# Performance work log

Measured on AMD Instinct MI355X. Metric: run time of the kernel, lower is better.

The kernel has to match this reference:

```python
import jax, jax.numpy as jnp
import numpy as np

D_MODEL = 1024
N_HEADS = 16
HEAD_DIM = D_MODEL // N_HEADS  # 64
TOP_K = 64
EPS = 1e-12  # matches F.normalize eps


def setup_inputs() -> dict:
    key = jax.random.key(0)
    ks = jax.random.split(key, 6)
    s = 0.02
    def w(k):
        return jax.random.normal(k, (D_MODEL, D_MODEL), jnp.float32) * s
    zb = jnp.zeros((D_MODEL,), jnp.float32)
    # x: (B, T, d_model); T must equal d_model (see compress_proj constraint)
    x = jax.random.normal(ks[0], (2, 1024, D_MODEL), jnp.float32)
    return {
        "x": x,
        "Wq": w(ks[1]), "bq": zb,
        "Wk": w(ks[2]), "bk": zb,
        "Wv": w(ks[3]), "bv": zb,
        "Wo": w(ks[4]), "bo": zb,
        "Wc": w(ks[5]), "bc": zb,  # compress_proj (applied along time axis)
    }


def _l2norm(a):
    n = jnp.linalg.norm(a, axis=-1, keepdims=True)
    return a / jnp.maximum(n, EPS)


def reference(x, Wq, bq, Wk, bk, Wv, bv, Wo, bo, Wc, bc):
    B, T, Dm = x.shape
    H, hd = N_HEADS, HEAD_DIM

    def proj(W, b):
        return (x @ W.T + b).reshape(B, T, H, hd).transpose(0, 2, 1, 3)  # (B,H,T,hd)

    Q = proj(Wq, bq)
    K = proj(Wk, bk)
    V = proj(Wv, bv)

    # compress_kv with compress_ratio=1: compress_proj acts on the (transposed)
    # time axis, so K_comp[b,h,c,d] = sum_t K[b,h,t,d] * Wc[c,t] + bc[c]
    K_comp = jnp.einsum('bhtd,ct->bhcd', K, Wc) + bc[None, None, :, None]
    V_comp = jnp.einsum('bhtd,ct->bhcd', V, Wc) + bc[None, None, :, None]

    # lightning indexer: cosine similarity + top-k over compressed slots
    sim = jnp.einsum('bhtd,bhcd->bhtc', _l2norm(Q), _l2norm(K_comp))
    topk_idx = jax.lax.top_k(sim, TOP_K)[1]  # (B,H,T,K)

    bi = jnp.arange(B)[:, None, None, None]
    hi = jnp.arange(H)[None, :, None, None]
    K_sel = K_comp[bi, hi, topk_idx]  # (B,H,T,K,hd)
    V_sel = V_comp[bi, hi, topk_idx]

    scores = jnp.einsum('bhtd,bhtkd->bhtk', Q, K_sel) / float(np.sqrt(hd))
    attn = jax.nn.softmax(scores, axis=-1)
    out = jnp.einsum('bhtk,bhtkd->bhtd', attn, V_sel)  # (B,H,T,hd)
    out = out.transpose(0, 2, 1, 3).reshape(B, T, Dm)
    return out @ Wo.T + bo
```

## Files before the change

kernel.cpp:

```cpp
#include <hip/hip_runtime.h>
#include <type_traits>


#define DEVI __device__ __forceinline__

constexpr int Tn = 1024;
constexpr int Cn = 1024;
constexpr int Hn = 16;

typedef short bf16x8 __attribute__((ext_vector_type(8)));
typedef float f32x4 __attribute__((ext_vector_type(4)));
typedef double f64x4 __attribute__((ext_vector_type(4)));

DEVI int wsumi(int v)   { for (int m = 1; m < 64; m <<= 1) v += __shfl_xor(v, m); return v; }
DEVI int wmini(int v)   { for (int m = 1; m < 64; m <<= 1) { int o = __shfl_xor(v, m); v = o < v ? o : v; } return v; }
DEVI float wfmax(float v){ for (int m = 1; m < 64; m <<= 1) v = fmaxf(v, __shfl_xor(v, m)); return v; }
DEVI float wfsum(float v){ for (int m = 1; m < 64; m <<= 1) v += __shfl_xor(v, m); return v; }

DEVI unsigned long long mapd(double x) {
  unsigned long long b = (unsigned long long)__double_as_longlong(x);
  return (b >> 63) ? ~b : (b | 0x8000000000000000ull);
}

DEVI unsigned short f2bf_rne(float x) {
  unsigned u = __float_as_uint(x);
  u += 0x7fffu + ((u >> 16) & 1u);
  return (unsigned short)(u >> 16);
}
struct BfPair { short hi, lo; };
DEVI BfPair split2(float x) {
  unsigned short h = f2bf_rne(x);
  float hf = __uint_as_float(((unsigned)h) << 16);
  BfPair r;
  r.hi = (short)h;
  r.lo = (short)f2bf_rne(x - hf);
  return r;
}

template <typename OUTT, bool BTRANS, int BIASMODE>
DEVI void f64_body(float* AsB, float* BsB,
    const float* Ab, const float* Bb, const float* bias, OUTT* Cb,
    int Kd, int lda, int ldb, int ldc, int m0, int n0)
{
  const int tid = threadIdx.x;
  const int lane = tid & 63, w = tid >> 6;
  const int wr = w >> 1, wc = w & 1;
  const int l15 = lane & 15, l4 = lane >> 4;

  f64x4 zz = {0.0, 0.0, 0.0, 0.0};
  f64x4 p1 = __builtin_amdgcn_mfma_f64_16x16x4f64(1.0, (double)l15, zz, 0, 0, 0);
  f64x4 p2 = __builtin_amdgcn_mfma_f64_16x16x4f64((double)l15, 1.0, zz, 0, 0, 0);
  int a1 = 1, b1 = 1, c1 = 1, a2 = 1, b2 = 1, c2 = 1;
#pragma unroll
  for (int rr = 0; rr < 4; ++rr) {
    a1 &= (p1[rr] == 4.0 * l15);
    b1 &= (p1[rr] == 4.0 * (l4 * 4 + rr));
    c1 &= (p1[rr] == 4.0 * (l4 + 4 * rr));
    a2 &= (p2[rr] == 4.0 * (l4 * 4 + rr));
    b2 &= (p2[rr] == 4.0 * (l4 + 4 * rr));
    c2 &= (p2[rr] == 4.0 * l15);
  }
  a1 = __all(a1); b1 = __all(b1); c1 = __all(c1);
  a2 = __all(a2); b2 = __all(b2); c2 = __all(c2);
  int dmap = 0, useM = 1;
  if      (a1 && a2) dmap = 0;
  else if (a1 && b2) dmap = 1;
  else if (b1 && c2) dmap = 2;
  else if (c1 && c2) dmap = 3;
  else useM = 0;

  f64x4 acc[2][2];
#pragma unroll
  for (int i = 0; i < 2; ++i)
#pragma unroll
    for (int j = 0; j < 2; ++j) acc[i][j] = (f64x4){0.0, 0.0, 0.0, 0.0};

  const int sm = tid >> 2, skf = tid & 3;
  const int bkl = tid >> 4, bnf = tid & 15;

  const int nT = Kd >> 5;
  float4 a0_, a1_, b0_, b1_;

  auto LOADT = [&](int k0) {
    a0_ = *(const float4*)(Ab + (size_t)(m0 + sm) * lda + k0 + 4 * skf);
    a1_ = *(const float4*)(Ab + (size_t)(m0 + sm) * lda + k0 + 16 + 4 * skf);
    if (BTRANS) {
      b0_ = *(const float4*)(Bb + (size_t)(n0 + sm) * ldb + k0 + 4 * skf);
      b1_ = *(const float4*)(Bb + (size_t)(n0 + sm) * ldb + k0 + 16 + 4 * skf);
    } else {
      b0_ = *(const float4*)(Bb + (size_t)(k0 + bkl) * ldb + n0 + 4 * bnf);
      b1_ = *(const float4*)(Bb + (size_t)(k0 + 16 + bkl) * ldb + n0 + 4 * bnf);
    }
  };
  auto WRITET = [&](int buf) {
    float* As = AsB + buf * 2304;
    float* Bs = BsB + buf * 2304;
    As[(4 * skf + 0) * 72 + sm] = a0_.x; As[(4 * skf + 1) * 72 + sm] = a0_.y;
    As[(4 * skf + 2) * 72 + sm] = a0_.z; As[(4 * skf + 3) * 72 + sm] = a0_.w;
    As[(16 + 4 * skf + 0) * 72 + sm] = a1_.x; As[(16 + 4 * skf + 1) * 72 + sm] = a1_.y;
    As[(16 + 4 * skf + 2) * 72 + sm] = a1_.z; As[(16 + 4 * skf + 3) * 72 + sm] = a1_.w;
    if (BTRANS) {
      Bs[(4 * skf + 0) * 72 + sm] = b0_.x; Bs[(4 * skf + 1) * 72 + sm] = b0_.y;
      Bs[(4 * skf + 2) * 72 + sm] = b0_.z; Bs[(4 * skf + 3) * 72 + sm] = b0_.w;
      Bs[(16 + 4 * skf + 0) * 72 + sm] = b1_.x; Bs[(16 + 4 * skf + 1) * 72 + sm] = b1_.y;
      Bs[(16 + 4 * skf + 2) * 72 + sm] = b1_.z; Bs[(16 + 4 * skf + 3) * 72 + sm] = b1_.w;
    } else {
      *(float4*)&Bs[bkl * 72 + 4 * bnf] = b0_;
      *(float4*)&Bs[(16 + bkl) * 72 + 4 * bnf] = b1_;
    }
  };

  LOADT(0);
  WRITET(0);
  __syncthreads();

  for (int kt = 0; kt < nT; ++kt) {
    const int cur = kt & 1;
    if (kt + 1 < nT) LOADT((kt + 1) * 32);

    const float* As = AsB + cur * 2304;
    const float* Bs = BsB + cur * 2304;
    if (useM) {
#pragma unroll
      for (int kq = 0; kq < 8; ++kq) {
        int kk = kq * 4 + l4;
        double a0  = (double)As[kk * 72 + wr * 32 + l15];
        double a1v = (double)As[kk * 72 + wr * 32 + 16 + l15];
        double b0  = (double)Bs[kk * 72 + wc * 32 + l15];
        double b1v = (double)Bs[kk * 72 + wc * 32 + 16 + l15];
        acc[0][0] = __builtin_amdgcn_mfma_f64_16x16x4f64(a0,  b0,  acc[0][0], 0, 0, 0);
        acc[0][1] = __builtin_amdgcn_mfma_f64_16x16x4f64(a0,  b1v, acc[0][1], 0, 0, 0);
        acc[1][0] = __builtin_amdgcn_mfma_f64_16x16x4f64(a1v, b0,  acc[1][0], 0, 0, 0);
        acc[1][1] = __builtin_amdgcn_mfma_f64_16x16x4f64(a1v, b1v, acc[1][1], 0, 0, 0);
      }
    } else {
#pragma unroll
      for (int k = 0; k < 32; ++k) {
        double bv0 = (double)Bs[k * 72 + wc * 32 + l15];
        double bv1 = (double)Bs[k * 72 + wc * 32 + 16 + l15];
#pragma unroll
        for (int fr = 0; fr < 2; ++fr)
#pragma unroll
          for (int rr = 0; rr < 4; ++rr) {
            double av = (double)As[k * 72 + wr * 32 + fr * 16 + l4 * 4 + rr];
            acc[fr][0][rr] += av * bv0;
            acc[fr][1][rr] += av * bv1;
          }
      }
    }

    if (kt + 1 < nT) WRITET(cur ^ 1);
    __syncthreads();
  }

#pragma unroll
  for (int fr = 0; fr < 2; ++fr)
#pragma unroll
    for (int fc = 0; fc < 2; ++fc)
#pragma unroll
      for (int rr = 0; rr < 4; ++rr) {
        int ri, ci;
        if (!useM || dmap == 0) { ri = l4 * 4 + rr; ci = l15; }
        else if (dmap == 1)     { ri = l4 + 4 * rr; ci = l15; }
        else if (dmap == 2)     { ri = l15; ci = l4 * 4 + rr; }
        else                    { ri = l15; ci = l4 + 4 * rr; }
        int row = m0 + wr * 32 + fr * 16 + ri;
        int col = n0 + wc * 32 + fc * 16 + ci;
        double v = acc[fr][fc][rr];
        if constexpr (std::is_same<OUTT, double>::value) {
          Cb[(size_t)row * ldc + col] = v;
        } else {
          float s = (float)v;
          float cb = (BIASMODE == 1) ? bias[col] : 0.f;
          float rb = (BIASMODE == 2) ? bias[row] : 0.f;
          ((float*)Cb)[(size_t)row * ldc + col] = s + cb + rb;
        }
      }
}

template <bool BTRANS, int BIASMODE>
DEVI void bf16_body(short* AhB, short* AlB, short* BhB, short* BlB,
    const float* A, const float* Bz, const float* bias, float* Cz,
    int Kd, int lda, int ldb, int ldc, int m0, int n0)
{
  const int tid = threadIdx.x;
  const int lane = tid & 63, w = tid >> 6;
  const int wr = w >> 1, wc = w & 1;
  const int r16 = lane & 15, kg = lane >> 4;

  f32x4 acc[2][2];
#pragma unroll
  for (int i = 0; i < 2; ++i)
#pragma unroll
    for (int j = 0; j < 2; ++j) acc[i][j] = (f32x4){0.f, 0.f, 0.f, 0.f};

  const int row = tid >> 2, kseg = tid & 3;
  const int gcol = tid & 63, gks = tid >> 6;

  const int nT = Kd >> 5;
  float4 pa0, pa1, pb0, pb1;
  float gb[8];

  auto LOADT = [&](int k0) {
    pa0 = *(const float4*)(A + (size_t)(m0 + row) * lda + k0 + kseg * 8);
    pa1 = *(const float4*)(A + (size_t)(m0 + row) * lda + k0 + kseg * 8 + 4);
    if (BTRANS) {
      pb0 = *(const float4*)(Bz + (size_t)(n0 + row) * ldb + k0 + kseg * 8);
      pb1 = *(const float4*)(Bz + (size_t)(n0 + row) * ldb + k0 + kseg * 8 + 4);
    } else {
#pragma unroll
      for (int j = 0; j < 8; ++j)
        gb[j] = Bz[(size_t)(k0 + gks * 8 + j) * ldb + n0 + gcol];
    }
  };
  auto WRITET = [&](int buf) {
    {
      BfPair q0 = split2(pa0.x), q1 = split2(pa0.y), q2 = split2(pa0.z), q3 = split2(pa0.w);
      BfPair q4 = split2(pa1.x), q5 = split2(pa1.y), q6 = split2(pa1.z), q7 = split2(pa1.w);
      bf16x8 h = {q0.hi, q1.hi, q2.hi, q3.hi, q4.hi, q5.hi, q6.hi, q7.hi};
      bf16x8 l = {q0.lo, q1.lo, q2.lo, q3.lo, q4.lo, q5.lo, q6.lo, q7.lo};
      int idx = (kseg * 64 + row) * 8;
      *(bf16x8*)&AhB[buf * 2048 + idx] = h;
      *(bf16x8*)&AlB[buf * 2048 + idx] = l;
    }
    if (BTRANS) {
      BfPair q0 = split2(pb0.x), q1 = split2(pb0.y), q2 = split2(pb0.z), q3 = split2(pb0.w);
      BfPair q4 = split2(pb1.x), q5 = split2(pb1.y), q6 = split2(pb1.z), q7 = split2(pb1.w);
      bf16x8 h = {q0.hi, q1.hi, q2.hi, q3.hi, q4.hi, q5.hi, q6.hi, q7.hi};
      bf16x8 l = {q0.lo, q1.lo, q2.lo, q3.lo, q4.lo, q5.lo, q6.lo, q7.lo};
      int idx = (kseg * 64 + row) * 8;
      *(bf16x8*)&BhB[buf * 2048 + idx] = h;
      *(bf16x8*)&BlB[buf * 2048 + idx] = l;
    } else {
      short hv[8], lv[8];
#pragma unroll
      for (int j = 0; j < 8; ++j) {
        BfPair p = split2(gb[j]);
        hv[j] = p.hi; lv[j] = p.lo;
      }
      bf16x8 h = {hv[0], hv[1], hv[2], hv[3], hv[4], hv[5], hv[6], hv[7]};
      bf16x8 l = {lv[0], lv[1], lv[2], lv[3], lv[4], lv[5], lv[6], lv[7]};
      int idx = (gks * 64 + gcol) * 8;
      *(bf16x8*)&BhB[buf * 2048 + idx] = h;
      *(bf16x8*)&BlB[buf * 2048 + idx] = l;
    }
  };

  LOADT(0);
  WRITET(0);
  __syncthreads();

  for (int kt = 0; kt < nT; ++kt) {
    const int cur = kt & 1;
    if (kt + 1 < nT) LOADT((kt + 1) * 32);

    bf16x8 ah[2], al[2], bh[2], bl[2];
#pragma unroll
    for (int f = 0; f < 2; ++f) {
      int ia = (kg * 64 + wr * 32 + f * 16 + r16) * 8;
      int ib = (kg * 64 + wc * 32 + f * 16 + r16) * 8;
      ah[f] = *(const bf16x8*)&AhB[cur * 2048 + ia];
      al[f] = *(const bf16x8*)&AlB[cur * 2048 + ia];
      bh[f] = *(const bf16x8*)&BhB[cur * 2048 + ib];
      bl[f] = *(const bf16x8*)&BlB[cur * 2048 + ib];
    }
#pragma unroll
    for (int fr = 0; fr < 2; ++fr)
#pragma unroll
      for (int fc = 0; fc < 2; ++fc) {
        f32x4 c = acc[fr][fc];
        c = __builtin_amdgcn_mfma_f32_16x16x32_bf16(al[fr], bh[fc], c, 0, 0, 0);
        c = __builtin_amdgcn_mfma_f32_16x16x32_bf16(ah[fr], bl[fc], c, 0, 0, 0);
        c = __builtin_amdgcn_mfma_f32_16x16x32_bf16(ah[fr], bh[fc], c, 0, 0, 0);
        acc[fr][fc] = c;
      }

    if (kt + 1 < nT) WRITET(cur ^ 1);
    __syncthreads();
  }

#pragma unroll
  for (int fr = 0; fr < 2; ++fr)
#pragma unroll
    for (int fc = 0; fc < 2; ++fc) {
      int col = n0 + wc * 32 + fc * 16 + r16;
      float cb = (BIASMODE == 1) ? bias[col] : 0.f;
#pragma unroll
      for (int rr = 0; rr < 4; ++rr) {
        int rw = m0 + wr * 32 + fr * 16 + kg * 4 + rr;
        float rb = (BIASMODE == 2) ? bias[rw] : 0.f;
        Cz[(size_t)rw * ldc + col] = acc[fr][fc][rr] + cb + rb;
      }
    }
}

__global__ __launch_bounds__(256) void projQKV_k(
    const float* __restrict__ x,
    const float* __restrict__ Wq, const float* __restrict__ Wk,
    const float* __restrict__ Wv,
    const float* __restrict__ bq, const float* __restrict__ bk,
    const float* __restrict__ bv,
    float* __restrict__ Q, float* __restrict__ Kf, float* __restrict__ Vf)
{
  __shared__ __align__(16) float S1[2 * 2304];
  __shared__ __align__(16) float S2[2 * 2304];
  const int m0 = blockIdx.y * 64, n0 = blockIdx.x * 64;
  if (blockIdx.z < 2) {
    const float* W = blockIdx.z ? Wk : Wq;
    const float* b = blockIdx.z ? bk : bq;
    float* C = blockIdx.z ? Kf : Q;
    f64_body<float, true, 1>(S1, S2, x, W, b, C, 1024, 1024, 1024, 1024, m0, n0);
  } else {
    bf16_body<true, 1>((short*)S1, (short*)S1 + 4096,
                       (short*)S2, (short*)S2 + 4096,
                       x, Wv, bv, Vf, 1024, 1024, 1024, 1024, m0, n0);
  }
}

__global__ __launch_bounds__(256) void compKV_k(
    const float* __restrict__ Wc, const float* __restrict__ Kf,
    const float* __restrict__ Vf, const float* __restrict__ bc,
    float* __restrict__ Kc, float* __restrict__ Vc)
{
  __shared__ __align__(16) float S1[2 * 2304];
  __shared__ __align__(16) float S2[2 * 2304];
  const int m0 = blockIdx.y * 64, n0 = blockIdx.x * 64;
  const size_t M1 = (size_t)1024 * 1024;
  if (blockIdx.z < 2) {
    f64_body<float, false, 2>(S1, S2, Wc, Kf + blockIdx.z * M1, bc,
                              Kc + blockIdx.z * M1, 1024, 1024, 1024, 1024, m0, n0);
  } else {
    int zb = blockIdx.z - 2;
    bf16_body<false, 2>((short*)S1, (short*)S1 + 4096,
                        (short*)S2, (short*)S2 + 4096,
                        Wc, Vf + zb * M1, bc, Vc + zb * M1,
                        1024, 1024, 1024, 1024, m0, n0);
  }
}

__global__ __launch_bounds__(256) void dotsim_k(
    const float* __restrict__ Q, const float* __restrict__ Kc,
    double* __restrict__ dotp, int group_base)
{
  __shared__ __align__(16) float S1[2 * 2304];
  __shared__ __align__(16) float S2[2 * 2304];
  const int m0 = blockIdx.y * 64, n0 = blockIdx.x * 64;
  int pair = group_base + (int)blockIdx.z;
  int bb = pair >> 4, hh = pair & 15;
  const float* Ab = Q + ((size_t)bb * Tn) * 1024 + (size_t)hh * 64;
  const float* Bb = Kc + ((size_t)bb * Cn) * 1024 + (size_t)hh * 64;
  double* Cb = dotp + (size_t)blockIdx.z * Tn * Cn;
  f64_body<double, true, 0>(S1, S2, Ab, Bb, nullptr, Cb, 64, 1024, 1024, 1024, m0, n0);
}

__global__ __launch_bounds__(256) void wo_k(
    const float* __restrict__ at, const float* __restrict__ Wo,
    const float* __restrict__ bo, float* __restrict__ out)
{
  __shared__ __align__(16) float S1[2 * 2304];
  __shared__ __align__(16) float S2[2 * 2304];
  const int m0 = blockIdx.y * 64, n0 = blockIdx.x * 64;
  bf16_body<true, 1>((short*)S1, (short*)S1 + 4096,
                     (short*)S2, (short*)S2 + 4096,
                     at, Wo, bo, out, 1024, 1024, 1024, 1024, m0, n0);
}

__global__ __launch_bounds__(256) void kn_k2(const float* __restrict__ Kc,
                                             double* __restrict__ kn)
{
  int idx = (int)blockIdx.x * 256 + (int)threadIdx.x;
  int c = idx & 1023;
  int p = idx >> 10;
  int b = p >> 4, h = p & 15;
  const float* row = Kc + ((size_t)(b * 1024 + c)) * 1024 + h * 64;
  double s = 0.0;
  for (int d = 0; d < 64; ++d) { double v = (double)row[d]; s += v * v; }
  kn[(size_t)p * 1024 + c] = 1.0 / fmax(sqrt(s), 1e-12);
}

__global__ __launch_bounds__(256) void topk_attn_k(
    const double* __restrict__ dotb, const double* __restrict__ kn,
    const float* __restrict__ Vc, float* __restrict__ attnout, int group_base)
{
  __shared__ int sC[4][64];
  __shared__ float sD[4][64];

  const int lane = threadIdx.x & 63, wv = threadIdx.x >> 6;
  const int g = (int)blockIdx.x >> 8;
  const int t = ((int)blockIdx.x & 255) * 4 + wv;
  const int pair = group_base + g;
  const int bb = pair >> 4, hh = pair & 15;

  const double* drow = dotb + ((size_t)g * Tn + t) * (size_t)Cn;
  const double* knr  = kn + ((size_t)(bb * Hn + hh)) * Cn;

  double dv[16];
  unsigned long long u[16];
#pragma unroll
  for (int j = 0; j < 8; ++j) {
    double2 dd = *(const double2*)(drow + j * 128 + 2 * lane);
    double2 kk = *(const double2*)(knr  + j * 128 + 2 * lane);
    dv[2 * j] = dd.x; dv[2 * j + 1] = dd.y;
    u[2 * j]     = mapd(dd.x * kk.x);
    u[2 * j + 1] = mapd(dd.y * kk.y);
  }
  unsigned hi[16];
#pragma unroll
  for (int i = 0; i < 16; ++i) hi[i] = (unsigned)(u[i] >> 32);

  unsigned TH = 0;
  for (int bit = 31; bit >= 0; --bit) {
    unsigned Tc = TH | (1u << bit);
    int c = 0;
#pragma unroll
    for (int i = 0; i < 16; ++i) c += (hi[i] >= Tc);
    if (wsumi(c) >= 64) TH = Tc;
  }
  int mhi = 0;
#pragma unroll
  for (int i = 0; i < 16; ++i) mhi += (hi[i] > TH);
  mhi = wsumi(mhi);
  const int need1 = 64 - mhi;
  unsigned TL = 0;
  for (int bit = 31; bit >= 0; --bit) {
    unsigned Tc = TL | (1u << bit);
    int c = 0;
#pragma unroll
    for (int i = 0; i < 16; ++i) c += (hi[i] == TH && (unsigned)u[i] >= Tc);
    if (wsumi(c) >= need1) TL = Tc;
  }
  const unsigned long long V64 = ((unsigned long long)TH << 32) | TL;

  int base = 0;
#pragma unroll
  for (int i = 0; i < 16; ++i) {
    const int cix = 128 * (i >> 1) + 2 * lane + (i & 1);
    bool sel = (u[i] > V64);
    unsigned long long mk = __ballot(sel);
    if (sel) {
      int r = __popcll(mk & ((1ull << lane) - 1ull));
      sC[wv][base + r] = cix;
      sD[wv][base + r] = (float)dv[i];
    }
    base += __popcll(mk);
  }
  const int need = 64 - base;
  unsigned taken = 0;
  for (int r = 0; r < need; ++r) {
    int mn = 0x7fffffff;
#pragma unroll
    for (int i = 0; i < 16; ++i) {
      int cix = 128 * (i >> 1) + 2 * lane + (i & 1);
      if (u[i] == V64 && !((taken >> i) & 1u)) mn = mn < cix ? mn : cix;
    }
    mn = wmini(mn);
#pragma unroll
    for (int i = 0; i < 16; ++i) {
      int cix = 128 * (i >> 1) + 2 * lane + (i & 1);
      if (u[i] == V64 && !((taken >> i) & 1u) && cix == mn) {
        taken |= 1u << i;
        sC[wv][base + r] = mn;
        sD[wv][base + r] = (float)dv[i];
      }
    }
  }
  __syncthreads();

  int ck = sC[wv][lane];
  float sc = sD[wv][lane] * 0.125f;
  float mx = wfmax(sc);
  float w = expf(sc - mx);
  float sw = wfsum(w);
  w /= sw;

  const float* Vb = Vc + (size_t)bb * ((size_t)Cn * 1024) + hh * 64 + lane;
  float acc = 0.f;
#pragma unroll 4
  for (int k = 0; k < 64; ++k) {
    int c = __shfl(ck, k);
    float wk = __shfl(w, k);
    acc = fmaf(wk, Vb[(size_t)c * 1024], acc);
  }
  attnout[((size_t)(bb * Tn + t)) * 1024 + hh * 64 + lane] = acc;
}

extern "C" void kernel_launch(void* const* d_in, const int* in_sizes, int n_in,
                              void* d_out, int out_size, void* d_ws, size_t ws_size,
                              hipStream_t stream)
{
  const float* x  = (const float*)d_in[0];
  const float* Wq = (const float*)d_in[1];
  const float* bq = (const float*)d_in[2];
  const float* Wk = (const float*)d_in[3];
  const float* bk = (const float*)d_in[4];
  const float* Wv = (const float*)d_in[5];
  const float* bv = (const float*)d_in[6];
  const float* Wo = (const float*)d_in[7];
  const float* bo = (const float*)d_in[8];
  const float* Wc = (const float*)d_in[9];
  const float* bc = (const float*)d_in[10];
  float* out = (float*)d_out;

  const size_t NE = (size_t)2048 * 1024;
  float* Q   = (float*)d_ws;
  float* Kf  = Q + NE;
  float* Vf  = Kf + NE;
  float* Kc  = Vf + NE;
  float* Vc  = Kc + NE;
  float* at  = Vc + NE;
  double* kn = (double*)(at + NE);
  double* tail = kn + 32768;

  const size_t fixedB = 6 * NE * 4 + 32768 * 8;
  const size_t dotPairB = (size_t)Tn * Cn * 8;
  if (ws_size < fixedB) return;

  size_t rem = ws_size - fixedB;
  double* dotp; int G;
  if      (rem >= 32 * dotPairB) { G = 32; dotp = tail; }
  else if (rem >= 16 * dotPairB) { G = 16; dotp = tail; }
  else if (rem >=  8 * dotPairB) { G = 8;  dotp = tail; }
  else if (rem >=  4 * dotPairB) { G = 4;  dotp = tail; }
  else if (rem >=  2 * dotPairB) { G = 2;  dotp = tail; }
  else { G = 2; dotp = (double*)Kf; }

  dim3 blk(256, 1, 1);

  projQKV_k<<<dim3(16, 32, 3), blk, 0, stream>>>(
      x, Wq, Wk, Wv, bq, bk, bv, Q, Kf, Vf);

  compKV_k<<<dim3(16, 16, 4), blk, 0, stream>>>(Wc, Kf, Vf, bc, Kc, Vc);

  kn_k2<<<dim3(128), blk, 0, stream>>>(Kc, kn);

  for (int gb = 0; gb < 32; gb += G) {
    dotsim_k<<<dim3(16, 16, G), blk, 0, stream>>>(Q, Kc, dotp, gb);
    topk_attn_k<<<dim3(256 * G), blk, 0, stream>>>(dotp, kn, Vc, at, gb);
  }

  wo_k<<<dim3(16, 32, 1), blk, 0, stream>>>(at, Wo, bo, out);
}
```

Measured before the change: 810.2 us.

## Software-pipeline dot-similarity GEMM with top-k attention in a fused kernel

Adds a combined kernel whose first 1024 blocks compute the f64 dot-similarity tiles for the next group of four (batch, head) pairs, while the remaining blocks run top-k selection and attention on the previous group from a double buffer. GEMM-bound and latency-bound work now share the GPU instead of running as alternating launches. The cost is a smaller group size, about eight launches where the largest workspace allowed two, and less cache locality. Small workspaces keep the old path, without its 8/16/32 group sizes.

```diff
diff --git a/kernel.cpp b/kernel.cpp
--- a/kernel.cpp
+++ b/kernel.cpp
@@ -294,6 +294,111 @@
     }
 }
 
+DEVI void topk_body(const double* __restrict__ dotb, const double* __restrict__ kn,
+                    const float* __restrict__ Vc, float* __restrict__ attnout,
+                    int flat, int group_base, int* sCp, float* sDp)
+{
+  const int lane = threadIdx.x & 63, wv = threadIdx.x >> 6;
+  const int g = flat >> 8;
+  const int t = (flat & 255) * 4 + wv;
+  const int pair = group_base + g;
+  const int bb = pair >> 4, hh = pair & 15;
+
+  const double* drow = dotb + ((size_t)g * Tn + t) * (size_t)Cn;
+  const double* knr  = kn + ((size_t)(bb * Hn + hh)) * Cn;
+  int* sC = sCp + wv * 64;
+  float* sD = sDp + wv * 64;
+
+  double dv[16];
+  unsigned long long u[16];
+#pragma unroll
+  for (int j = 0; j < 8; ++j) {
+    double2 dd = *(const double2*)(drow + j * 128 + 2 * lane);
+    double2 kk = *(const double2*)(knr  + j * 128 + 2 * lane);
+    dv[2 * j] = dd.x; dv[2 * j + 1] = dd.y;
+    u[2 * j]     = mapd(dd.x * kk.x);
+    u[2 * j + 1] = mapd(dd.y * kk.y);
+  }
+  unsigned hi[16];
+#pragma unroll
+  for (int i = 0; i < 16; ++i) hi[i] = (unsigned)(u[i] >> 32);
+
+  unsigned TH = 0;
+  for (int bit = 31; bit >= 0; --bit) {
+    unsigned Tc = TH | (1u << bit);
+    int c = 0;
+#pragma unroll
+    for (int i = 0; i < 16; ++i) c += (hi[i] >= Tc);
+    if (wsumi(c) >= 64) TH = Tc;
+  }
+  int mhi = 0;
+#pragma unroll
+  for (int i = 0; i < 16; ++i) mhi += (hi[i] > TH);
+  mhi = wsumi(mhi);
+  const int need1 = 64 - mhi;
+  unsigned TL = 0;
+  for (int bit = 31; bit >= 0; --bit) {
+    unsigned Tc = TL | (1u << bit);
+    int c = 0;
+#pragma unroll
+    for (int i = 0; i < 16; ++i) c += (hi[i] == TH && (unsigned)u[i] >= Tc);
+    if (wsumi(c) >= need1) TL = Tc;
+  }
+  const unsigned long long V64 = ((unsigned long long)TH << 32) | TL;
+
+  int base = 0;
+#pragma unroll
+  for (int i = 0; i < 16; ++i) {
+    const int cix = 128 * (i >> 1) + 2 * lane + (i & 1);
+    bool sel = (u[i] > V64);
+    unsigned long long mk = __ballot(sel);
+    if (sel) {
+      int r = __popcll(mk & ((1ull << lane) - 1ull));
+      sC[base + r] = cix;
+      sD[base + r] = (float)dv[i];
+    }
+    base += __popcll(mk);
+  }
+  const int need = 64 - base;
+  unsigned taken = 0;
+  for (int r = 0; r < need; ++r) {
+    int mn = 0x7fffffff;
+#pragma unroll
+    for (int i = 0; i < 16; ++i) {
+      int cix = 128 * (i >> 1) + 2 * lane + (i & 1);
+      if (u[i] == V64 && !((taken >> i) & 1u)) mn = mn < cix ? mn : cix;
+    }
+    mn = wmini(mn);
+#pragma unroll
+    for (int i = 0; i < 16; ++i) {
+      int cix = 128 * (i >> 1) + 2 * lane + (i & 1);
+      if (u[i] == V64 && !((taken >> i) & 1u) && cix == mn) {
+        taken |= 1u << i;
+        sC[base + r] = mn;
+        sD[base + r] = (float)dv[i];
+      }
+    }
+  }
+  __syncthreads();
+
+  int ck = sC[lane];
+  float sc = sD[lane] * 0.125f;
+  float mx = wfmax(sc);
+  float w = expf(sc - mx);
+  float sw = wfsum(w);
+  w /= sw;
+
+  const float* Vb = Vc + (size_t)bb * ((size_t)Cn * 1024) + hh * 64 + lane;
+  float acc = 0.f;
+#pragma unroll 4
+  for (int k = 0; k < 64; ++k) {
+    int c = __shfl(ck, k);
+    float wk = __shfl(w, k);
+    acc = fmaf(wk, Vb[(size_t)c * 1024], acc);
+  }
+  attnout[((size_t)(bb * Tn + t)) * 1024 + hh * 64 + lane] = acc;
+}
+
 __global__ __launch_bounds__(256) void projQKV_k(
     const float* __restrict__ x,
     const float* __restrict__ Wq, const float* __restrict__ Wk,
@@ -353,16 +458,36 @@
   f64_body<double, true, 0>(S1, S2, Ab, Bb, nullptr, Cb, 64, 1024, 1024, 1024, m0, n0);
 }
 
-__global__ __launch_bounds__(256) void wo_k(
-    const float* __restrict__ at, const float* __restrict__ Wo,
-    const float* __restrict__ bo, float* __restrict__ out)
+__global__ __launch_bounds__(256) void topk_attn_k(
+    const double* __restrict__ dotb, const double* __restrict__ kn,
+    const float* __restrict__ Vc, float* __restrict__ attnout, int group_base)
+{
+  __shared__ int sC[4 * 64];
+  __shared__ float sD[4 * 64];
+  topk_body(dotb, kn, Vc, attnout, (int)blockIdx.x, group_base, sC, sD);
+}
+
+__global__ __launch_bounds__(256) void pipe_k(
+    const float* __restrict__ Q, const float* __restrict__ Kc,
+    const double* __restrict__ kn, const float* __restrict__ Vc,
+    float* __restrict__ at, const double* __restrict__ dcur,
+    double* __restrict__ dnext, int gcur_base, int gnext_base)
 {
   __shared__ __align__(16) float S1[2 * 2304];
   __shared__ __align__(16) float S2[2 * 2304];
-  const int m0 = blockIdx.y * 64, n0 = blockIdx.x * 64;
-  bf16_body<true, 1>((short*)S1, (short*)S1 + 4096,
-                     (short*)S2, (short*)S2 + 4096,
-                     at, Wo, bo, out, 1024, 1024, 1024, 1024, m0, n0);
+  const int flat = (int)blockIdx.x;
+  if (flat < 1024) {
+    int z = flat >> 8, r = flat & 255;
+    int m0 = (r >> 4) * 64, n0 = (r & 15) * 64;
+    int pair = gnext_base + z;
+    int bb = pair >> 4, hh = pair & 15;
+    const float* Ab = Q + ((size_t)bb * Tn) * 1024 + (size_t)hh * 64;
+    const float* Bb = Kc + ((size_t)bb * Cn) * 1024 + (size_t)hh * 64;
+    double* Cb = dnext + (size_t)z * Tn * Cn;
+    f64_body<double, true, 0>(S1, S2, Ab, Bb, nullptr, Cb, 64, 1024, 1024, 1024, m0, n0);
+  } else {
+    topk_body(dcur, kn, Vc, at, flat - 1024, gcur_base, (int*)S1, (float*)S2);
+  }
 }
 
 __global__ __launch_bounds__(256) void kn_k2(const float* __restrict__ Kc,
@@ -378,110 +503,16 @@
   kn[(size_t)p * 1024 + c] = 1.0 / fmax(sqrt(s), 1e-12);
 }
 
-__global__ __launch_bounds__(256) void topk_attn_k(
-    const double* __restrict__ dotb, const double* __restrict__ kn,
-    const float* __restrict__ Vc, float* __restrict__ attnout, int group_base)
-{
-  __shared__ int sC[4][64];
-  __shared__ float sD[4][64];
-
-  const int lane = threadIdx.x & 63, wv = threadIdx.x >> 6;
-  const int g = (int)blockIdx.x >> 8;
-  const int t = ((int)blockIdx.x & 255) * 4 + wv;
-  const int pair = group_base + g;
-  const int bb = pair >> 4, hh = pair & 15;
-
-  const double* drow = dotb + ((size_t)g * Tn + t) * (size_t)Cn;
-  const double* knr  = kn + ((size_t)(bb * Hn + hh)) * Cn;
-
-  double dv[16];
-  unsigned long long u[16];
-#pragma unroll
-  for (int j = 0; j < 8; ++j) {
-    double2 dd = *(const double2*)(drow + j * 128 + 2 * lane);
-    double2 kk = *(const double2*)(knr  + j * 128 + 2 * lane);
-    dv[2 * j] = dd.x; dv[2 * j + 1] = dd.y;
-    u[2 * j]     = mapd(dd.x * kk.x);
-    u[2 * j + 1] = mapd(dd.y * kk.y);
-  }
-  unsigned hi[16];
-#pragma unroll
-  for (int i = 0; i < 16; ++i) hi[i] = (unsigned)(u[i] >> 32);
-
-  unsigned TH = 0;
-  for (int bit = 31; bit >= 0; --bit) {
-    unsigned Tc = TH | (1u << bit);
-    int c = 0;
-#pragma unroll
-    for (int i = 0; i < 16; ++i) c += (hi[i] >= Tc);
-    if (wsumi(c) >= 64) TH = Tc;
-  }
-  int mhi = 0;
-#pragma unroll
-  for (int i = 0; i < 16; ++i) mhi += (hi[i] > TH);
-  mhi = wsumi(mhi);
-  const int need1 = 64 - mhi;
-  unsigned TL = 0;
-  for (int bit = 31; bit >= 0; --bit) {
-    unsigned Tc = TL | (1u << bit);
-    int c = 0;
-#pragma unroll
-    for (int i = 0; i < 16; ++i) c += (hi[i] == TH && (unsigned)u[i] >= Tc);
-    if (wsumi(c) >= need1) TL = Tc;
-  }
-  const unsigned long long V64 = ((unsigned long long)TH << 32) | TL;
-
-  int base = 0;
-#pragma unroll
-  for (int i = 0; i < 16; ++i) {
-    const int cix = 128 * (i >> 1) + 2 * lane + (i & 1);
-    bool sel = (u[i] > V64);
-    unsigned long long mk = __ballot(sel);
-    if (sel) {
-      int r = __popcll(mk & ((1ull << lane) - 1ull));
-      sC[wv][base + r] = cix;
-      sD[wv][base + r] = (float)dv[i];
-    }
-    base += __popcll(mk);
-  }
-  const int need = 64 - base;
-  unsigned taken = 0;
-  for (int r = 0; r < need; ++r) {
-    int mn = 0x7fffffff;
-#pragma unroll
-    for (int i = 0; i < 16; ++i) {
-      int cix = 128 * (i >> 1) + 2 * lane + (i & 1);
-      if (u[i] == V64 && !((taken >> i) & 1u)) mn = mn < cix ? mn : cix;
-    }
-    mn = wmini(mn);
-#pragma unroll
-    for (int i = 0; i < 16; ++i) {
-      int cix = 128 * (i >> 1) + 2 * lane + (i & 1);
-      if (u[i] == V64 && !((taken >> i) & 1u) && cix == mn) {
-        taken |= 1u << i;
-        sC[wv][base + r] = mn;
-        sD[wv][base + r] = (float)dv[i];
-      }
-    }
-  }
-  __syncthreads();
-
-  int ck = sC[wv][lane];
-  float sc = sD[wv][lane] * 0.125f;
-  float mx = wfmax(sc);
-  float w = expf(sc - mx);
-  float sw = wfsum(w);
-  w /= sw;
-
-  const float* Vb = Vc + (size_t)bb * ((size_t)Cn * 1024) + hh * 64 + lane;
-  float acc = 0.f;
-#pragma unroll 4
-  for (int k = 0; k < 64; ++k) {
-    int c = __shfl(ck, k);
-    float wk = __shfl(w, k);
-    acc = fmaf(wk, Vb[(size_t)c * 1024], acc);
-  }
-  attnout[((size_t)(bb * Tn + t)) * 1024 + hh * 64 + lane] = acc;
+__global__ __launch_bounds__(256) void wo_k(
+    const float* __restrict__ at, const float* __restrict__ Wo,
+    const float* __restrict__ bo, float* __restrict__ out)
+{
+  __shared__ __align__(16) float S1[2 * 2304];
+  __shared__ __align__(16) float S2[2 * 2304];
+  const int m0 = blockIdx.y * 64, n0 = blockIdx.x * 64;
+  bf16_body<true, 1>((short*)S1, (short*)S1 + 4096,
+                     (short*)S2, (short*)S2 + 4096,
+                     at, Wo, bo, out, 1024, 1024, 1024, 1024, m0, n0);
 }
 
 extern "C" void kernel_launch(void* const* d_in, const int* in_sizes, int n_in,
@@ -515,15 +546,6 @@
   const size_t dotPairB = (size_t)Tn * Cn * 8;
   if (ws_size < fixedB) return;
 
-  size_t rem = ws_size - fixedB;
-  double* dotp; int G;
-  if      (rem >= 32 * dotPairB) { G = 32; dotp = tail; }
-  else if (rem >= 16 * dotPairB) { G = 16; dotp = tail; }
-  else if (rem >=  8 * dotPairB) { G = 8;  dotp = tail; }
-  else if (rem >=  4 * dotPairB) { G = 4;  dotp = tail; }
-  else if (rem >=  2 * dotPairB) { G = 2;  dotp = tail; }
-  else { G = 2; dotp = (double*)Kf; }
-
   dim3 blk(256, 1, 1);
 
   projQKV_k<<<dim3(16, 32, 3), blk, 0, stream>>>(
@@ -533,9 +555,27 @@
 
   kn_k2<<<dim3(128), blk, 0, stream>>>(Kc, kn);
 
-  for (int gb = 0; gb < 32; gb += G) {
-    dotsim_k<<<dim3(16, 16, G), blk, 0, stream>>>(Q, Kc, dotp, gb);
-    topk_attn_k<<<dim3(256 * G), blk, 0, stream>>>(dotp, kn, Vc, at, gb);
+  size_t rem = ws_size - fixedB;
+  const size_t planeElems = (size_t)4 * Tn * Cn;
+
+  if (rem >= 8 * dotPairB) {
+    double* bufs[2] = { tail, tail + planeElems };
+    dotsim_k<<<dim3(16, 16, 4), blk, 0, stream>>>(Q, Kc, bufs[0], 0);
+    for (int g = 0; g < 7; ++g) {
+      pipe_k<<<dim3(2048), blk, 0, stream>>>(
+          Q, Kc, kn, Vc, at, bufs[g & 1], bufs[(g + 1) & 1],
+          g * 4, (g + 1) * 4);
+    }
+    topk_attn_k<<<dim3(1024), blk, 0, stream>>>(bufs[1], kn, Vc, at, 28);
+  } else {
+    double* dotp; int G;
+    if      (rem >= 4 * dotPairB) { G = 4; dotp = tail; }
+    else if (rem >= 2 * dotPairB) { G = 2; dotp = tail; }
+    else { G = 2; dotp = (double*)Kf; }
+    for (int gb = 0; gb < 32; gb += G) {
+      dotsim_k<<<dim3(16, 16, G), blk, 0, stream>>>(Q, Kc, dotp, gb);
+      topk_attn_k<<<dim3(256 * G), blk, 0, stream>>>(dotp, kn, Vc, at, gb);
+    }
   }
 
   wo_k<<<dim3(16, 32, 1), blk, 0, stream>>>(at, Wo, bo, out);
```

Result: slower. 1.025 ms (+26.5%).
